# Optimization experiments

Hardware: AMD Instinct MI355X
Metric: run time of the kernel (lower is better)

The kernel has to match this reference:

```python
import jax, jax.numpy as jnp
import numpy as np

HEADS = 8
DIM_HEAD = 64
DIM = 512
B, N = 4, 2048
SCALE = DIM_HEAD ** -0.5


def setup_inputs() -> dict:
    key = jax.random.key(0)
    k1, k2, k3, k4, k5, k6 = jax.random.split(key, 6)
    inner = HEADS * DIM_HEAD
    s = DIM ** -0.5
    return {
        "input_feature": jax.random.normal(k1, (B, N, DIM), dtype=jnp.float32),
        "mask": jax.random.randint(k2, (B, N), 0, 2, dtype=jnp.int32),
        "Wq": jax.random.normal(k3, (inner, DIM), dtype=jnp.float32) * s,
        "Wk": jax.random.normal(k4, (inner, DIM), dtype=jnp.float32) * s,
        "Wv": jax.random.normal(k5, (inner, DIM), dtype=jnp.float32) * s,
        "Wout": jax.random.normal(k6, (DIM, inner), dtype=jnp.float32) * s,
    }


def reference(input_feature, mask, Wq, Wk, Wv, Wout):
    # Conv1d with kernel_size=1, no bias == per-token linear: out = W @ x_channels
    q = jnp.einsum('bnc,dc->bnd', input_feature, Wq)  # [B, N, H*Dh]
    k = jnp.einsum('bnc,dc->bnd', input_feature, Wk)
    v = jnp.einsum('bnc,dc->bnd', input_feature, Wv)

    # '(n c)' channel layout is head-major -> reshape to [B, N, H, Dh], move head out front
    def split_heads(t):
        return t.reshape(B, N, HEADS, DIM_HEAD).transpose(2, 0, 1, 3)  # [H, B, N, Dh]

    q, k, v = split_heads(q), split_heads(k), split_heads(v)

    scores = jnp.einsum('hbtd,hbsd->hbts', q, k) * SCALE  # [H, B, N, N]
    # masked_fill(mask == 0, 1e-9): fill with small CONSTANT (not -inf), faithful to source
    m = (mask == 0)[None, :, None, :]  # [1, B, 1, N]
    scores = jnp.where(m, jnp.float32(1e-9), scores)
    att = jax.nn.softmax(scores, axis=-1)
    out = jnp.einsum('hbts,hbsd->hbtd', att, v)  # [H, B, N, Dh]

    # '(n b) tokens c -> b (n c) tokens' : head-major channel concat
    out = out.transpose(1, 2, 0, 3).reshape(B, N, HEADS * DIM_HEAD)  # [B, N, H*Dh]
    out = jnp.einsum('bnd,ed->bne', out, Wout)  # [B, N, DIM]
    return out
```

## Files before the change

### kernel.cpp

```cpp
#include <hip/hip_runtime.h>
#include <hip/hip_bf16.h>

typedef __attribute__((ext_vector_type(8))) short short8;
typedef __attribute__((ext_vector_type(4))) short short4_t;
typedef __attribute__((ext_vector_type(4))) float float4_;

#define LOG2E 1.4426950408889634f

__device__ __forceinline__ short f2bf(float f) {
    unsigned int u = __builtin_bit_cast(unsigned int, f);
    u = (u + 0x7FFFu + ((u >> 16) & 1u)) >> 16;
    return (short)u;
}

__device__ __forceinline__ unsigned pk2bf(float a, float b) {
    unsigned ua = __builtin_bit_cast(unsigned, a) + 0x8000u;
    unsigned ub = __builtin_bit_cast(unsigned, b) + 0x8000u;
    return __builtin_amdgcn_perm(ub, ua, 0x07060302);
}

__device__ __forceinline__ void gload_lds16(const short* g, short* l) {
    __builtin_amdgcn_global_load_lds((const __attribute__((address_space(1))) void*)g,
                                     (__attribute__((address_space(3))) void*)l, 16, 0, 0);
}

__global__ __launch_bounds__(256) void cvt_kernel(
    const float* __restrict__ X, const float* __restrict__ Wq, const float* __restrict__ Wk,
    const float* __restrict__ Wv, const float* __restrict__ Wo,
    short* __restrict__ Xb, short* __restrict__ Wqkvb, short* __restrict__ Wob) {
    int i = blockIdx.x * 256 + threadIdx.x;
    const float* src; short* dst; float sc = 1.0f;
    if (i < 1048576) { src = X + (size_t)i * 4; dst = Xb + (size_t)i * 4; }
    else {
        int w = i - 1048576; int sec = w >> 16; int j = (w & 65535) * 4;
        if (sec == 0)      { src = Wq + j; dst = Wqkvb + j; sc = 0.125f * LOG2E; }
        else if (sec == 1) { src = Wk + j; dst = Wqkvb + 262144 + j; }
        else if (sec == 2) { src = Wv + j; dst = Wqkvb + 524288 + j; }
        else               { src = Wo + j; dst = Wob + j; }
    }
    float4 v = *(const float4*)src;
    short4_t o;
    o[0] = f2bf(v.x * sc); o[1] = f2bf(v.y * sc); o[2] = f2bf(v.z * sc); o[3] = f2bf(v.w * sc);
    *(short4_t*)dst = o;
}

__global__ __launch_bounds__(256) void gemm_qkv(const short* __restrict__ A, const short* __restrict__ B,
                                                const int* __restrict__ mask,
                                                short* __restrict__ Qb, short* __restrict__ Kb,
                                                short* __restrict__ Vtb) {
    __shared__ short At[128 * 64];
    __shared__ short Bt[128 * 64];
    __shared__ int maskL[128];
    constexpr int K = 512;
    int tid = threadIdx.x;
    int wid = tid >> 6, lane = tid & 63;
    int quad = lane >> 4, cc = lane & 15;
    int c7 = cc & 7;
    int wr = wid >> 1, wc = wid & 1;
    int m0 = blockIdx.y * 128, n0 = blockIdx.x * 128;
    if (tid < 128) maskL[tid] = mask[m0 + tid];

    float4_ acc[4][4] = {};

    for (int kk = 0; kk < K; kk += 64) {
#pragma unroll
        for (int p = 0; p < 4; ++p) {
            int slot = p * 256 + tid;
            int r = slot >> 3, c = slot & 7;
            int cs = (c ^ (r & 7)) * 8;
            gload_lds16(A + (size_t)(m0 + r) * K + kk + cs, At + slot * 8);
            gload_lds16(B + (size_t)(n0 + r) * K + kk + cs, Bt + slot * 8);
        }
        __syncthreads();
#pragma unroll
        for (int kc = 0; kc < 2; ++kc) {
            short8 af[4], bf[4];
#pragma unroll
            for (int i = 0; i < 4; ++i)
                af[i] = *(const short8*)(At + (wr * 64 + i * 16 + cc) * 64 + (((kc * 4 + quad) ^ c7) * 8));
#pragma unroll
            for (int j = 0; j < 4; ++j)
                bf[j] = *(const short8*)(Bt + (wc * 64 + j * 16 + cc) * 64 + (((kc * 4 + quad) ^ c7) * 8));
#pragma unroll
            for (int i = 0; i < 4; ++i)
#pragma unroll
                for (int j = 0; j < 4; ++j)
                    acc[i][j] = __builtin_amdgcn_mfma_f32_16x16x32_bf16(af[i], bf[j], acc[i][j], 0, 0, 0);
        }
        __syncthreads();
    }

    int which = n0 >> 9;
    int b = m0 >> 11;
    if (which == 2) {
#pragma unroll
        for (int i = 0; i < 4; ++i) {
#pragma unroll
            for (int j = 0; j < 4; ++j) {
                int d = (n0 & 511) + wc * 64 + j * 16 + cc;
                int nn = (m0 & 2047) + wr * 64 + i * 16 + quad * 4;
                short4_t pv;
                pv[0] = f2bf(acc[i][j][0]); pv[1] = f2bf(acc[i][j][1]);
                pv[2] = f2bf(acc[i][j][2]); pv[3] = f2bf(acc[i][j][3]);
                *(short4_t*)(Vtb + ((size_t)(b * 512 + d)) * 2048 + nn) = pv;
            }
        }
    } else {
        short* dst = which ? Kb : Qb;
#pragma unroll
        for (int i = 0; i < 4; ++i) {
#pragma unroll
            for (int j = 0; j < 4; ++j) {
#pragma unroll
                for (int r = 0; r < 4; ++r) {
                    int lm = wr * 64 + i * 16 + quad * 4 + r;
                    int nn = (m0 & 2047) + lm;
                    int hd = (n0 & 511) + wc * 64 + j * 16 + cc;
                    int h = hd >> 6, dh = hd & 63;
                    float v = acc[i][j][r];
                    if (which == 1 && maskL[lm] == 0) v = 0.0f;
                    dst[((((size_t)b * 8 + h) * 2048 + nn) * 64) + dh] = f2bf(v);
                }
            }
        }
    }
}

__global__ __launch_bounds__(256) void attn_kernel(const short* __restrict__ Q, const short* __restrict__ Kg,
                                                   const short* __restrict__ Vt,
                                                   short* __restrict__ AO) {
    __shared__ __align__(16) char smem[40960];
    short* KbufL = (short*)smem;
    short* VbufL = (short*)(smem + 16384);
    short* Pt    = (short*)(smem + 32768);
    float* Lw    = (float*)smem;
    float* Lfin  = (float*)(smem + 1024);

    int tid = threadIdx.x;
    int w = tid >> 6, lane = tid & 63;
    int quad = lane >> 4, cc = lane & 15;
    int tg = w >> 1, dh = w & 1;
    int bh = blockIdx.x, b = bh >> 3, h = bh & 7;
    int t0 = blockIdx.y * 64;
    size_t kbase = (size_t)bh * 2048 * 64;
    size_t vbase = (size_t)b * 512 * 2048 + (size_t)h * 64 * 2048;

    short8 qf[4][2];
#pragma unroll
    for (int tb = 0; tb < 4; ++tb)
#pragma unroll
        for (int kc = 0; kc < 2; ++kc)
            qf[tb][kc] = *(const short8*)(Q + kbase + (size_t)(t0 + tb * 16 + cc) * 64 + kc * 32 + quad * 8);

    int c7 = cc & 7;
    int koff[2], poff_w[4], aoff[2][2], voff[2][2];
#pragma unroll
    for (int kc = 0; kc < 2; ++kc)
        koff[kc] = (w * 16 + cc) * 64 + (((kc * 4 + quad) ^ c7) * 8);
#pragma unroll
    for (int tb = 0; tb < 4; ++tb)
        poff_w[tb] = (tb * 16 + cc) * 64 + (((w * 2 + (quad >> 1)) ^ c7) * 8) + (quad & 1) * 4;
#pragma unroll
    for (int mb = 0; mb < 2; ++mb)
#pragma unroll
        for (int kc = 0; kc < 2; ++kc)
            aoff[mb][kc] = (tg * 32 + mb * 16 + cc) * 64 + (((kc * 4 + quad) ^ c7) * 8);
#pragma unroll
    for (int db = 0; db < 2; ++db)
#pragma unroll
        for (int kc = 0; kc < 2; ++kc)
            voff[db][kc] = (dh * 32 + db * 16 + cc) * 64 + (((kc * 4 + quad) ^ c7) * 8);

    float4_ o[2][2] = {};
    float lp[4] = {0.f, 0.f, 0.f, 0.f};

#pragma unroll
    for (int pass = 0; pass < 4; ++pass) {
        int slot = pass * 256 + tid;
        if (slot < 512) {
            int s = slot >> 3, c = slot & 7;
            gload_lds16(Kg + kbase + (size_t)s * 64 + ((c ^ (s & 7)) * 8), KbufL + slot * 8);
        } else {
            int q = slot - 512;
            int d = q >> 3, c = q & 7;
            gload_lds16(Vt + vbase + (size_t)d * 2048 + ((c ^ (d & 7)) * 8), VbufL + q * 8);
        }
    }

    for (int it = 0; it < 32; ++it) {
        int cur = it & 1;
        const short* Kt  = KbufL + cur * 4096;
        const short* Vtt = VbufL + cur * 4096;
        __syncthreads();

        if (it < 31) {
            int s1 = (it + 1) * 64;
            short* Kn = KbufL + (cur ^ 1) * 4096;
            short* Vn = VbufL + (cur ^ 1) * 4096;
#pragma unroll
            for (int pass = 0; pass < 4; ++pass) {
                int slot = pass * 256 + tid;
                if (slot < 512) {
                    int s = slot >> 3, c = slot & 7;
                    gload_lds16(Kg + kbase + (size_t)(s1 + s) * 64 + ((c ^ (s & 7)) * 8), Kn + slot * 8);
                } else {
                    int q = slot - 512;
                    int d = q >> 3, c = q & 7;
                    gload_lds16(Vt + vbase + (size_t)d * 2048 + s1 + ((c ^ (d & 7)) * 8), Vn + q * 8);
                }
            }
        }

        short8 kf0 = *(const short8*)(Kt + koff[0]);
        short8 kf1 = *(const short8*)(Kt + koff[1]);
        float4_ acc[4];
#pragma unroll
        for (int tb = 0; tb < 4; ++tb) {
            float4_ a = {0.f, 0.f, 0.f, 0.f};
            a = __builtin_amdgcn_mfma_f32_16x16x32_bf16(kf0, qf[tb][0], a, 0, 0, 0);
            a = __builtin_amdgcn_mfma_f32_16x16x32_bf16(kf1, qf[tb][1], a, 0, 0, 0);
            acc[tb] = a;
        }
#pragma unroll
        for (int tb = 0; tb < 4; ++tb) {
            float x0 = __builtin_amdgcn_exp2f(acc[tb][0]);
            float x1 = __builtin_amdgcn_exp2f(acc[tb][1]);
            float x2 = __builtin_amdgcn_exp2f(acc[tb][2]);
            float x3 = __builtin_amdgcn_exp2f(acc[tb][3]);
            lp[tb] += (x0 + x1) + (x2 + x3);
            uint2 pw; pw.x = pk2bf(x0, x1); pw.y = pk2bf(x2, x3);
            *(uint2*)(Pt + poff_w[tb]) = pw;
        }
        __syncthreads();

        short8 af[2][2], vf[2][2];
#pragma unroll
        for (int mb = 0; mb < 2; ++mb)
#pragma unroll
            for (int kc = 0; kc < 2; ++kc)
                af[mb][kc] = *(const short8*)(Pt + aoff[mb][kc]);
#pragma unroll
        for (int db = 0; db < 2; ++db)
#pragma unroll
            for (int kc = 0; kc < 2; ++kc)
                vf[db][kc] = *(const short8*)(Vtt + voff[db][kc]);
#pragma unroll
        for (int mb = 0; mb < 2; ++mb)
#pragma unroll
            for (int db = 0; db < 2; ++db) {
                o[mb][db] = __builtin_amdgcn_mfma_f32_16x16x32_bf16(af[mb][0], vf[db][0], o[mb][db], 0, 0, 0);
                o[mb][db] = __builtin_amdgcn_mfma_f32_16x16x32_bf16(af[mb][1], vf[db][1], o[mb][db], 0, 0, 0);
            }
    }

#pragma unroll
    for (int tb = 0; tb < 4; ++tb) {
        lp[tb] += __shfl_xor(lp[tb], 16, 64);
        lp[tb] += __shfl_xor(lp[tb], 32, 64);
    }
    __syncthreads();
    if (lane < 16) {
#pragma unroll
        for (int tb = 0; tb < 4; ++tb) Lw[w * 64 + tb * 16 + lane] = lp[tb];
    }
    __syncthreads();
    if (tid < 64) {
        float s = Lw[tid] + Lw[64 + tid] + Lw[128 + tid] + Lw[192 + tid];
        Lfin[tid] = 1.0f / s;
    }
    __syncthreads();

#pragma unroll
    for (int mb = 0; mb < 2; ++mb)
#pragma unroll
        for (int r = 0; r < 4; ++r) {
            int tl = tg * 32 + mb * 16 + quad * 4 + r;
            float inv = Lfin[tl];
            size_t rowbase = ((size_t)(b * 2048 + t0 + tl)) * 512 + h * 64;
#pragma unroll
            for (int db = 0; db < 2; ++db)
                AO[rowbase + dh * 32 + db * 16 + cc] = f2bf(o[mb][db][r] * inv);
        }
}

__global__ __launch_bounds__(256) void gemm_out(const short* __restrict__ A, const short* __restrict__ B,
                                                float* __restrict__ C) {
    __shared__ short At[64 * 64];
    __shared__ short Bt[64 * 64];
    constexpr int K = 512;
    int tid = threadIdx.x;
    int wid = tid >> 6, lane = tid & 63;
    int quad = lane >> 4, cc = lane & 15;
    int c7 = cc & 7;
    int wr = wid >> 1, wc = wid & 1;
    int m0 = blockIdx.y * 64, n0 = blockIdx.x * 64;

    float4_ acc[2][2] = {};

    for (int kk = 0; kk < K; kk += 64) {
#pragma unroll
        for (int p = 0; p < 2; ++p) {
            int slot = p * 256 + tid;
            int r = slot >> 3, c = slot & 7;
            int cs = (c ^ (r & 7)) * 8;
            gload_lds16(A + (size_t)(m0 + r) * K + kk + cs, At + slot * 8);
            gload_lds16(B + (size_t)(n0 + r) * K + kk + cs, Bt + slot * 8);
        }
        __syncthreads();
#pragma unroll
        for (int kc = 0; kc < 2; ++kc) {
            short8 af[2], bf[2];
#pragma unroll
            for (int i = 0; i < 2; ++i)
                af[i] = *(const short8*)(At + (wr * 32 + i * 16 + cc) * 64 + (((kc * 4 + quad) ^ c7) * 8));
#pragma unroll
            for (int j = 0; j < 2; ++j)
                bf[j] = *(const short8*)(Bt + (wc * 32 + j * 16 + cc) * 64 + (((kc * 4 + quad) ^ c7) * 8));
#pragma unroll
            for (int i = 0; i < 2; ++i)
#pragma unroll
                for (int j = 0; j < 2; ++j)
                    acc[i][j] = __builtin_amdgcn_mfma_f32_16x16x32_bf16(af[i], bf[j], acc[i][j], 0, 0, 0);
        }
        __syncthreads();
    }

#pragma unroll
    for (int i = 0; i < 2; ++i)
#pragma unroll
        for (int j = 0; j < 2; ++j)
#pragma unroll
            for (int r = 0; r < 4; ++r) {
                int gm = m0 + wr * 32 + i * 16 + quad * 4 + r;
                int gn = n0 + wc * 32 + j * 16 + cc;
                C[(size_t)gm * 512 + gn] = acc[i][j][r];
            }
}

extern "C" void kernel_launch(void* const* d_in, const int* in_sizes, int n_in,
                              void* d_out, int out_size, void* d_ws, size_t ws_size,
                              hipStream_t stream) {
    const float* X  = (const float*)d_in[0];
    const int* mask = (const int*)d_in[1];
    const float* Wq = (const float*)d_in[2];
    const float* Wk = (const float*)d_in[3];
    const float* Wv = (const float*)d_in[4];
    const float* Wo = (const float*)d_in[5];

    char* ws = (char*)d_ws;
    short* Xbf   = (short*)(ws + 0);
    short* Wqkvb = (short*)(ws + 8388608);
    short* Wob   = (short*)(ws + 9961472);
    short* Qb    = (short*)(ws + 10485760);
    short* Kb    = (short*)(ws + 18874368);
    short* Vtb   = (short*)(ws + 27262976);
    short* AOb   = (short*)(ws + 35651584);

    cvt_kernel<<<5120, 256, 0, stream>>>(X, Wq, Wk, Wv, Wo, Xbf, Wqkvb, Wob);
    gemm_qkv<<<dim3(12, 64), 256, 0, stream>>>(Xbf, Wqkvb, mask, Qb, Kb, Vtb);
    attn_kernel<<<dim3(32, 32), 256, 0, stream>>>(Qb, Kb, Vtb, AOb);
    gemm_out<<<dim3(8, 128), 256, 0, stream>>>(AOb, Wob, (float*)d_out);
}
```

Baseline: 174.4 us.

## Prefetch K/V tiles through registers two steps ahead instead of direct-to-LDS loads

Replaces the global_load_lds direct-to-LDS copies of K and V tiles with ordinary vector loads into registers, issued two iterations ahead and written to the alternate LDS buffer one iteration later. Pointer increments replace the per-iteration address recomputation. It also adds a minimum-occupancy hint of 4 to the launch bounds. The aim is to hide global latency better, at the cost of extra VGPRs and explicit LDS store instructions.

```diff
diff --git a/kernel.cpp b/kernel.cpp
--- a/kernel.cpp
+++ b/kernel.cpp
@@ -126,9 +126,9 @@
     }
 }
 
-__global__ __launch_bounds__(256) void attn_kernel(const short* __restrict__ Q, const short* __restrict__ Kg,
-                                                   const short* __restrict__ Vt,
-                                                   short* __restrict__ AO) {
+__global__ __launch_bounds__(256, 4) void attn_kernel(const short* __restrict__ Q, const short* __restrict__ Kg,
+                                                      const short* __restrict__ Vt,
+                                                      short* __restrict__ AO) {
     __shared__ __align__(16) char smem[40960];
     short* KbufL = (short*)smem;
     short* VbufL = (short*)(smem + 16384);
@@ -174,18 +174,21 @@
     float4_ o[2][2] = {};
     float lp[4] = {0.f, 0.f, 0.f, 0.f};
 
-#pragma unroll
-    for (int pass = 0; pass < 4; ++pass) {
-        int slot = pass * 256 + tid;
-        if (slot < 512) {
-            int s = slot >> 3, c = slot & 7;
-            gload_lds16(Kg + kbase + (size_t)s * 64 + ((c ^ (s & 7)) * 8), KbufL + slot * 8);
-        } else {
-            int q = slot - 512;
-            int d = q >> 3, c = q & 7;
-            gload_lds16(Vt + vbase + (size_t)d * 2048 + ((c ^ (d & 7)) * 8), VbufL + q * 8);
-        }
-    }
+    int sA = tid >> 3, cA = tid & 7;
+    const short* gK0 = Kg + kbase + (size_t)sA * 64 + ((cA ^ (sA & 7)) * 8);
+    const short* gK1 = gK0 + 32 * 64;
+    const short* gV0 = Vt + vbase + (size_t)sA * 2048 + ((cA ^ (sA & 7)) * 8);
+    const short* gV1 = gV0 + 32 * 2048;
+    int ld0 = tid * 8, ld1 = tid * 8 + 2048;
+
+    short8 krg0 = *(const short8*)gK0, krg1 = *(const short8*)gK1;
+    short8 vrg0 = *(const short8*)gV0, vrg1 = *(const short8*)gV1;
+    gK0 += 4096; gK1 += 4096; gV0 += 64; gV1 += 64;
+    *(short8*)(KbufL + ld0) = krg0; *(short8*)(KbufL + ld1) = krg1;
+    *(short8*)(VbufL + ld0) = vrg0; *(short8*)(VbufL + ld1) = vrg1;
+    krg0 = *(const short8*)gK0; krg1 = *(const short8*)gK1;
+    vrg0 = *(const short8*)gV0; vrg1 = *(const short8*)gV1;
+    gK0 += 4096; gK1 += 4096; gV0 += 64; gV1 += 64;
 
     for (int it = 0; it < 32; ++it) {
         int cur = it & 1;
@@ -194,21 +197,15 @@
         __syncthreads();
 
         if (it < 31) {
-            int s1 = (it + 1) * 64;
             short* Kn = KbufL + (cur ^ 1) * 4096;
             short* Vn = VbufL + (cur ^ 1) * 4096;
-#pragma unroll
-            for (int pass = 0; pass < 4; ++pass) {
-                int slot = pass * 256 + tid;
-                if (slot < 512) {
-                    int s = slot >> 3, c = slot & 7;
-                    gload_lds16(Kg + kbase + (size_t)(s1 + s) * 64 + ((c ^ (s & 7)) * 8), Kn + slot * 8);
-                } else {
-                    int q = slot - 512;
-                    int d = q >> 3, c = q & 7;
-                    gload_lds16(Vt + vbase + (size_t)d * 2048 + s1 + ((c ^ (d & 7)) * 8), Vn + q * 8);
-                }
-            }
+            *(short8*)(Kn + ld0) = krg0; *(short8*)(Kn + ld1) = krg1;
+            *(short8*)(Vn + ld0) = vrg0; *(short8*)(Vn + ld1) = vrg1;
+        }
+        if (it < 30) {
+            krg0 = *(const short8*)gK0; krg1 = *(const short8*)gK1;
+            vrg0 = *(const short8*)gV0; vrg1 = *(const short8*)gV1;
+            gK0 += 4096; gK1 += 4096; gV0 += 64; gV1 += 64;
         }
 
         short8 kf0 = *(const short8*)(Kt + koff[0]);
```

Measured after the change: 166.4 us. 4.6% less time.
